# Kernel optimization log

Measured on AMD Instinct MI355X. Metric: run time of the kernel, lower is better.

The kernel has to match this reference:

```python
import jax, jax.numpy as jnp
import numpy as np

N_NODES = 50000
N_EDGES = 800000
IN_FEATS, H_FEATS, N_CLASSES = 64, 64, 16


def setup_inputs() -> dict:
    key = jax.random.key(0)
    ks = jax.random.split(key, 8)
    x = jax.random.normal(ks[0], (N_NODES, IN_FEATS), dtype=jnp.float32)
    src = jax.random.randint(ks[1], (N_EDGES,), 0, N_NODES, dtype=jnp.int64)
    dst = jax.random.randint(ks[2], (N_EDGES,), 0, N_NODES, dtype=jnp.int64)
    W_self1 = jax.random.normal(ks[3], (IN_FEATS, H_FEATS), dtype=jnp.float32) / np.sqrt(IN_FEATS)
    W_neigh1 = jax.random.normal(ks[4], (IN_FEATS, H_FEATS), dtype=jnp.float32) / np.sqrt(IN_FEATS)
    b1 = jnp.zeros((H_FEATS,), dtype=jnp.float32)
    W_self2 = jax.random.normal(ks[5], (H_FEATS, N_CLASSES), dtype=jnp.float32) / np.sqrt(H_FEATS)
    W_neigh2 = jax.random.normal(ks[6], (H_FEATS, N_CLASSES), dtype=jnp.float32) / np.sqrt(H_FEATS)
    b2 = jnp.zeros((N_CLASSES,), dtype=jnp.float32)
    return {"x": x, "src": src, "dst": dst,
            "W_self1": W_self1, "W_neigh1": W_neigh1, "b1": b1,
            "W_self2": W_self2, "W_neigh2": W_neigh2, "b2": b2}


def _mean_agg(h, src, dst, n_nodes):
    # gather source-node features along edges, sum into destinations, divide by in-degree
    summed = jax.ops.segment_sum(h[src], dst, num_segments=n_nodes)  # [N, d]
    deg = jax.ops.segment_sum(jnp.ones_like(src, dtype=h.dtype), dst, num_segments=n_nodes)
    return summed / jnp.maximum(deg, 1.0)[:, None]  # zero in-degree -> zeros (DGL semantics)


def _sage_layer(h, src, dst, W_self, W_neigh, b):
    h_neigh = _mean_agg(h, src, dst, h.shape[0])
    return h @ W_self + h_neigh @ W_neigh + b


def reference(x, src, dst, W_self1, W_neigh1, b1, W_self2, W_neigh2, b2):
    h = _sage_layer(x, src, dst, W_self1, W_neigh1, b1)
    h = jax.nn.relu(h)
    out = _sage_layer(h, src, dst, W_self2, W_neigh2, b2)
    return out
```

## Files before the change

kernel.cpp:

```cpp
#include <hip/hip_runtime.h>
#include <hip/hip_bf16.h>
#include <cstring>


#define FEATS 64
#define CLS   16
#define EPT   16
#define CAP   5120

typedef unsigned short bf16_t;
typedef float floatx2 __attribute__((ext_vector_type(2)));

__device__ __forceinline__ float bfbits2f(unsigned lo16) {
    unsigned v = lo16 << 16;
    float f;
    __builtin_memcpy(&f, &v, 4);
    return f;
}
__device__ __forceinline__ bf16_t f2bf(float f) {
    unsigned u;
    __builtin_memcpy(&u, &f, 4);
    u = (u + 0x7FFFu + ((u >> 16) & 1u)) >> 16;
    return (bf16_t)u;
}
__device__ __forceinline__ unsigned pack2(float a, float b) {
    return (unsigned)f2bf(a) | ((unsigned)f2bf(b) << 16);
}
__device__ __forceinline__ unsigned pack4_fp8(float a, float b, float c, float d) {
    int q = __builtin_amdgcn_cvt_pk_fp8_f32(a, b, 0, false);
    q = __builtin_amdgcn_cvt_pk_fp8_f32(c, d, q, true);
    return (unsigned)q;
}

__global__ __launch_bounds__(256) void fused_pg_kernel(
    const int* __restrict__ src, const int* __restrict__ dst,
    int* __restrict__ bucket_cnt, int* __restrict__ epart, int E,
    const float* __restrict__ x, const float* __restrict__ Ws,
    const float* __restrict__ Wn, bf16_t* __restrict__ selfo,
    unsigned char* __restrict__ t1, int N, int nbp)
{
    __shared__ float smem[16512];
    int t = threadIdx.x;

    if ((int)blockIdx.x < nbp) {
        int* hist = (int*)smem;
        int* base = hist + 256;
        int e0 = blockIdx.x * (256 * EPT);
        hist[t] = 0;
        __syncthreads();
        int pk[EPT];
        int bk[EPT];
#pragma unroll
        for (int j = 0; j < EPT; ++j) {
            int e = e0 + j * 256 + t;
            if (e < E) {
                int d = dst[e];
                pk[j] = (src[e] << 8) | (d & 255);
                bk[j] = d >> 8;
                atomicAdd(&hist[bk[j]], 1);
            } else bk[j] = -1;
        }
        __syncthreads();
        int c = hist[t];
        if (c) base[t] = atomicAdd(&bucket_cnt[t], c);
        hist[t] = 0;
        __syncthreads();
#pragma unroll
        for (int j = 0; j < EPT; ++j) {
            if (bk[j] >= 0) {
                int r = atomicAdd(&hist[bk[j]], 1);
                epart[bk[j] * CAP + base[bk[j]] + r] = pk[j];
            }
        }
        return;
    }

    float* Wc = smem;
    float* xs = smem + 8192;
    int node0 = ((int)blockIdx.x - nbp) * 128;

    for (int idx = t; idx < 64 * 128; idx += 256) {
        int k = idx >> 7, c = idx & 127;
        Wc[idx] = (c < 64) ? Ws[k * 64 + c] : Wn[k * 64 + (c - 64)];
    }
    for (int idx = t; idx < 128 * 16; idx += 256) {
        int row = idx >> 4, c4 = idx & 15;
        int node = node0 + row;
        float4 v = (node < N) ? ((const float4*)(x + (size_t)node * 64))[c4]
                              : make_float4(0.f, 0.f, 0.f, 0.f);
        float* p = &xs[row * 65 + c4 * 4];
        p[0] = v.x; p[1] = v.y; p[2] = v.z; p[3] = v.w;
    }
    __syncthreads();

    int m = t & 31;
    int g = t >> 5;
    float acc[4][16];
#pragma unroll
    for (int j = 0; j < 4; ++j)
#pragma unroll
        for (int c = 0; c < 16; ++c) acc[j][c] = 0.f;

    for (int k = 0; k < 64; ++k) {
        float w[16];
        const float* wp = &Wc[k * 128 + g * 16];
#pragma unroll
        for (int c = 0; c < 16; ++c) w[c] = wp[c];
        float a0 = xs[m * 65 + k];
        float a1 = xs[(m + 32) * 65 + k];
        float a2 = xs[(m + 64) * 65 + k];
        float a3 = xs[(m + 96) * 65 + k];
#pragma unroll
        for (int c = 0; c < 16; ++c) {
            acc[0][c] += a0 * w[c];
            acc[1][c] += a1 * w[c];
            acc[2][c] += a2 * w[c];
            acc[3][c] += a3 * w[c];
        }
    }
#pragma unroll
    for (int j = 0; j < 4; ++j) {
        int node = node0 + m + 32 * j;
        if (node < N) {
            if (g < 4) {
                bf16_t* dstp = selfo + (size_t)node * 64 + g * 16;
                uint4 p0, p1;
                p0.x = pack2(acc[j][0],  acc[j][1]);  p0.y = pack2(acc[j][2],  acc[j][3]);
                p0.z = pack2(acc[j][4],  acc[j][5]);  p0.w = pack2(acc[j][6],  acc[j][7]);
                p1.x = pack2(acc[j][8],  acc[j][9]);  p1.y = pack2(acc[j][10], acc[j][11]);
                p1.z = pack2(acc[j][12], acc[j][13]); p1.w = pack2(acc[j][14], acc[j][15]);
                *(uint4*)(dstp) = p0;
                *(uint4*)(dstp + 8) = p1;
            } else {
                unsigned char* dstp = t1 + (size_t)node * 64 + (g - 4) * 16;
                uint4 q;
                q.x = pack4_fp8(acc[j][0],  acc[j][1],  acc[j][2],  acc[j][3]);
                q.y = pack4_fp8(acc[j][4],  acc[j][5],  acc[j][6],  acc[j][7]);
                q.z = pack4_fp8(acc[j][8],  acc[j][9],  acc[j][10], acc[j][11]);
                q.w = pack4_fp8(acc[j][12], acc[j][13], acc[j][14], acc[j][15]);
                *(uint4*)(dstp) = q;
            }
        }
    }
}

__global__ __launch_bounds__(512) void buildcsr_kernel(const int* __restrict__ epart,
                                                       const int* __restrict__ bucket_cnt,
                                                       int* __restrict__ row_start,
                                                       unsigned short* __restrict__ deg16,
                                                       int* __restrict__ csr, int N) {
    __shared__ int cnt[256];
    __shared__ int pref[256];
    __shared__ int s[256];
    int t = threadIdx.x;
    int b = blockIdx.x;
    int ebeg = b * CAP;
    int ecnt = bucket_cnt[b];
    if (t < 256) cnt[t] = 0;
    __syncthreads();
    for (int e = t; e < ecnt; e += 512)
        atomicAdd(&cnt[epart[ebeg + e] & 255], 1);
    __syncthreads();
    int v = 0;
    if (t < 256) { v = cnt[t]; s[t] = v; }
    __syncthreads();
    for (int off = 1; off < 256; off <<= 1) {
        int u = (t < 256 && t >= off) ? s[t - off] : 0;
        __syncthreads();
        if (t < 256) s[t] += u;
        __syncthreads();
    }
    if (t < 256) {
        pref[t] = s[t] - v;
        int node = b * 256 + t;
        if (node < N) {
            row_start[node] = ebeg + pref[t];
            deg16[node] = (unsigned short)v;
        }
        cnt[t] = 0;
    }
    __syncthreads();
    for (int e = t; e < ecnt; e += 512) {
        int pk = epart[ebeg + e];
        int ln = pk & 255;
        int r = atomicAdd(&cnt[ln], 1);
        csr[ebeg + pref[ln] + r] = pk >> 8;
    }
}

__global__ __launch_bounds__(256) void gather64_kernel(
    const int* __restrict__ csr, const int* __restrict__ row_start,
    const unsigned short* __restrict__ deg16,
    const unsigned char* __restrict__ t1, const bf16_t* __restrict__ selfo,
    bf16_t* __restrict__ h1, const float* __restrict__ b1, int N)
{
    int wid = (blockIdx.x * 256 + threadIdx.x) >> 6;
    int lane = threadIdx.x & 63;
    int eslot = lane >> 3;
    int cg = lane & 7;
    if (wid >= N) return;
    int beg = row_start[wid];
    int d = deg16[wid];
    float a[8];
#pragma unroll
    for (int c = 0; c < 8; ++c) a[c] = 0.f;
    int i = eslot;
    for (; i + 8 < d; i += 16) {
        int s0 = csr[beg + i];
        int s1 = csr[beg + i + 8];
        uint2 r0 = *(const uint2*)(t1 + (size_t)s0 * 64 + cg * 8);
        uint2 r1 = *(const uint2*)(t1 + (size_t)s1 * 64 + cg * 8);
        floatx2 p0 = __builtin_amdgcn_cvt_pk_f32_fp8((int)r0.x, false);
        floatx2 p1 = __builtin_amdgcn_cvt_pk_f32_fp8((int)r0.x, true);
        floatx2 p2 = __builtin_amdgcn_cvt_pk_f32_fp8((int)r0.y, false);
        floatx2 p3 = __builtin_amdgcn_cvt_pk_f32_fp8((int)r0.y, true);
        floatx2 q0 = __builtin_amdgcn_cvt_pk_f32_fp8((int)r1.x, false);
        floatx2 q1 = __builtin_amdgcn_cvt_pk_f32_fp8((int)r1.x, true);
        floatx2 q2 = __builtin_amdgcn_cvt_pk_f32_fp8((int)r1.y, false);
        floatx2 q3 = __builtin_amdgcn_cvt_pk_f32_fp8((int)r1.y, true);
        a[0] += p0.x + q0.x;  a[1] += p0.y + q0.y;
        a[2] += p1.x + q1.x;  a[3] += p1.y + q1.y;
        a[4] += p2.x + q2.x;  a[5] += p2.y + q2.y;
        a[6] += p3.x + q3.x;  a[7] += p3.y + q3.y;
    }
    if (i < d) {
        int s0 = csr[beg + i];
        uint2 r0 = *(const uint2*)(t1 + (size_t)s0 * 64 + cg * 8);
        floatx2 p0 = __builtin_amdgcn_cvt_pk_f32_fp8((int)r0.x, false);
        floatx2 p1 = __builtin_amdgcn_cvt_pk_f32_fp8((int)r0.x, true);
        floatx2 p2 = __builtin_amdgcn_cvt_pk_f32_fp8((int)r0.y, false);
        floatx2 p3 = __builtin_amdgcn_cvt_pk_f32_fp8((int)r0.y, true);
        a[0] += p0.x; a[1] += p0.y; a[2] += p1.x; a[3] += p1.y;
        a[4] += p2.x; a[5] += p2.y; a[6] += p3.x; a[7] += p3.y;
    }
#pragma unroll
    for (int c = 0; c < 8; ++c) {
        a[c] += __shfl_xor(a[c], 8);
        a[c] += __shfl_xor(a[c], 16);
        a[c] += __shfl_xor(a[c], 32);
    }
    if (eslot == 0) {
        float inv = 1.f / fmaxf((float)d, 1.f);
        size_t o = (size_t)wid * 64 + cg * 8;
        uint4 su = *(const uint4*)(selfo + o);
        float4 b0 = *(const float4*)(b1 + cg * 8);
        float4 b4 = *(const float4*)(b1 + cg * 8 + 4);
        float r0 = fmaxf(bfbits2f(su.x & 0xffff) + a[0] * inv + b0.x, 0.f);
        float r1 = fmaxf(bfbits2f(su.x >> 16)    + a[1] * inv + b0.y, 0.f);
        float r2 = fmaxf(bfbits2f(su.y & 0xffff) + a[2] * inv + b0.z, 0.f);
        float r3 = fmaxf(bfbits2f(su.y >> 16)    + a[3] * inv + b0.w, 0.f);
        float r4 = fmaxf(bfbits2f(su.z & 0xffff) + a[4] * inv + b4.x, 0.f);
        float r5 = fmaxf(bfbits2f(su.z >> 16)    + a[5] * inv + b4.y, 0.f);
        float r6 = fmaxf(bfbits2f(su.w & 0xffff) + a[6] * inv + b4.z, 0.f);
        float r7 = fmaxf(bfbits2f(su.w >> 16)    + a[7] * inv + b4.w, 0.f);
        uint4 pk;
        pk.x = pack2(r0, r1);
        pk.y = pack2(r2, r3);
        pk.z = pack2(r4, r5);
        pk.w = pack2(r6, r7);
        *(uint4*)(h1 + o) = pk;
    }
}

__global__ __launch_bounds__(256) void gemm2_kernel(
    const bf16_t* __restrict__ h1, const float* __restrict__ Ws,
    const float* __restrict__ Wn, float* __restrict__ outp,
    bf16_t* __restrict__ t2, int N)
{
    __shared__ float Wc[64 * 32];
    __shared__ float xs[128 * 65];
    int t = threadIdx.x;
    int node0 = blockIdx.x * 128;

    for (int idx = t; idx < 64 * 32; idx += 256) {
        int k = idx >> 5, c = idx & 31;
        Wc[idx] = (c < 16) ? Ws[k * 16 + c] : Wn[k * 16 + (c - 16)];
    }
    for (int idx = t; idx < 128 * 8; idx += 256) {
        int row = idx >> 3, c8 = idx & 7;
        int node = node0 + row;
        float* p = &xs[row * 65 + c8 * 8];
        if (node < N) {
            uint4 u = *(const uint4*)(h1 + (size_t)node * 64 + c8 * 8);
            p[0] = bfbits2f(u.x & 0xffff); p[1] = bfbits2f(u.x >> 16);
            p[2] = bfbits2f(u.y & 0xffff); p[3] = bfbits2f(u.y >> 16);
            p[4] = bfbits2f(u.z & 0xffff); p[5] = bfbits2f(u.z >> 16);
            p[6] = bfbits2f(u.w & 0xffff); p[7] = bfbits2f(u.w >> 16);
        } else {
            for (int qq = 0; qq < 8; ++qq) p[qq] = 0.f;
        }
    }
    __syncthreads();

    int m = t & 31;
    int g = t >> 5;
    float acc[4][4];
#pragma unroll
    for (int j = 0; j < 4; ++j)
#pragma unroll
        for (int c = 0; c < 4; ++c) acc[j][c] = 0.f;

    for (int k = 0; k < 64; ++k) {
        float w[4];
        const float* wp = &Wc[k * 32 + g * 4];
#pragma unroll
        for (int c = 0; c < 4; ++c) w[c] = wp[c];
        float a0 = xs[m * 65 + k];
        float a1 = xs[(m + 32) * 65 + k];
        float a2 = xs[(m + 64) * 65 + k];
        float a3 = xs[(m + 96) * 65 + k];
#pragma unroll
        for (int c = 0; c < 4; ++c) {
            acc[0][c] += a0 * w[c];
            acc[1][c] += a1 * w[c];
            acc[2][c] += a2 * w[c];
            acc[3][c] += a3 * w[c];
        }
    }
#pragma unroll
    for (int j = 0; j < 4; ++j) {
        int node = node0 + m + 32 * j;
        if (node < N) {
            if (g < 4) {
                *(float4*)(outp + (size_t)node * 16 + g * 4) =
                    make_float4(acc[j][0], acc[j][1], acc[j][2], acc[j][3]);
            } else {
                uint2 pk;
                pk.x = pack2(acc[j][0], acc[j][1]);
                pk.y = pack2(acc[j][2], acc[j][3]);
                *(uint2*)(t2 + (size_t)node * 16 + (g - 4) * 4) = pk;
            }
        }
    }
}

__global__ __launch_bounds__(256) void gather16_kernel(
    const int* __restrict__ csr, const int* __restrict__ row_start,
    const unsigned short* __restrict__ deg16,
    const bf16_t* __restrict__ t2,
    float* __restrict__ outp, const float* __restrict__ b2, int N)
{
    int wid = (blockIdx.x * 256 + threadIdx.x) >> 6;
    int lane = threadIdx.x & 63;
    int eslot = lane >> 2;
    int cg = lane & 3;
    if (wid >= N) return;
    int beg = row_start[wid];
    int d = deg16[wid];
    float a0 = 0.f, a1 = 0.f, a2 = 0.f, a3 = 0.f;
    for (int i = eslot; i < d; i += 16) {
        int s0 = csr[beg + i];
        uint2 u = *(const uint2*)(t2 + (size_t)s0 * 16 + cg * 4);
        a0 += bfbits2f(u.x & 0xffff);
        a1 += bfbits2f(u.x >> 16);
        a2 += bfbits2f(u.y & 0xffff);
        a3 += bfbits2f(u.y >> 16);
    }
    a0 += __shfl_xor(a0, 4); a1 += __shfl_xor(a1, 4);
    a2 += __shfl_xor(a2, 4); a3 += __shfl_xor(a3, 4);
    a0 += __shfl_xor(a0, 8); a1 += __shfl_xor(a1, 8);
    a2 += __shfl_xor(a2, 8); a3 += __shfl_xor(a3, 8);
    a0 += __shfl_xor(a0, 16); a1 += __shfl_xor(a1, 16);
    a2 += __shfl_xor(a2, 16); a3 += __shfl_xor(a3, 16);
    a0 += __shfl_xor(a0, 32); a1 += __shfl_xor(a1, 32);
    a2 += __shfl_xor(a2, 32); a3 += __shfl_xor(a3, 32);
    if (eslot == 0) {
        float inv = 1.f / fmaxf((float)d, 1.f);
        size_t o = (size_t)wid * 16 + cg * 4;
        float4 bb = *(const float4*)(b2 + cg * 4);
        float4 ov = *(const float4*)(outp + o);
        ov.x += a0 * inv + bb.x;
        ov.y += a1 * inv + bb.y;
        ov.z += a2 * inv + bb.z;
        ov.w += a3 * inv + bb.w;
        *(float4*)(outp + o) = ov;
    }
}

extern "C" void kernel_launch(void* const* d_in, const int* in_sizes, int n_in,
                              void* d_out, int out_size, void* d_ws, size_t ws_size,
                              hipStream_t stream) {
    const float* x   = (const float*)d_in[0];
    const int*   src = (const int*)d_in[1];
    const int*   dst = (const int*)d_in[2];
    const float* Ws1 = (const float*)d_in[3];
    const float* Wn1 = (const float*)d_in[4];
    const float* b1  = (const float*)d_in[5];
    const float* Ws2 = (const float*)d_in[6];
    const float* Wn2 = (const float*)d_in[7];
    const float* b2  = (const float*)d_in[8];
    float* outp = (float*)d_out;

    const int N = in_sizes[0] / FEATS;
    const int E = in_sizes[1];
    const int B = (N + 255) / 256;
    const int NBP = (E + 256 * EPT - 1) / (256 * EPT);
    const int NBG = (N + 127) / 128;

    char* p = (char*)d_ws;
    auto align16 = [](char* q) { return (char*)(((size_t)q + 15) & ~(size_t)15); };
    int* bucket_cnt    = (int*)p;                  p = (char*)(bucket_cnt + 256);
    int* epart         = (int*)p;                  p = (char*)(epart + (size_t)B * CAP);
    int* csr           = (int*)p;                  p = (char*)(csr + (size_t)B * CAP);
    int* row_start     = (int*)align16(p);         p = (char*)(row_start + N);
    unsigned short* deg16 = (unsigned short*)align16(p); p = (char*)(deg16 + N);
    bf16_t* selfo      = (bf16_t*)align16(p);      p = (char*)(selfo + (size_t)N * 64);
    unsigned char* t1  = (unsigned char*)align16(p); p = (char*)(t1 + (size_t)N * 64);
    bf16_t* h1         = (bf16_t*)align16(p);      p = (char*)(h1 + (size_t)N * 64);
    bf16_t* t2         = (bf16_t*)align16(p);

    hipMemsetAsync(bucket_cnt, 0, 256 * sizeof(int), stream);

    fused_pg_kernel<<<NBP + NBG, 256, 0, stream>>>(
        src, dst, bucket_cnt, epart, E, x, Ws1, Wn1, selfo, t1, N, NBP);
    buildcsr_kernel<<<B, 512, 0, stream>>>(epart, bucket_cnt, row_start, deg16, csr, N);

    gather64_kernel<<<((size_t)N * 64 + 255) / 256, 256, 0, stream>>>(
        csr, row_start, deg16, t1, selfo, h1, b1, N);
    gemm2_kernel<<<(N + 127) / 128, 256, 0, stream>>>(h1, Ws2, Wn2, outp, t2, N);
    gather16_kernel<<<((size_t)N * 64 + 255) / 256, 256, 0, stream>>>(
        csr, row_start, deg16, t2, outp, b2, N);
}
```

Measured before the change: 162.2 us.

## Fuse layer-2 GEMM into layer-1 gather kernel via wave shuffles

```diff
diff --git a/kernel.cpp b/kernel.cpp
--- a/kernel.cpp
+++ b/kernel.cpp
@@ -188,22 +188,35 @@
     }
 }
 
-__global__ __launch_bounds__(256) void gather64_kernel(
+__global__ __launch_bounds__(256) void gather64g2_kernel(
     const int* __restrict__ csr, const int* __restrict__ row_start,
     const unsigned short* __restrict__ deg16,
     const unsigned char* __restrict__ t1, const bf16_t* __restrict__ selfo,
-    bf16_t* __restrict__ h1, const float* __restrict__ b1, int N)
+    const float* __restrict__ b1,
+    const float* __restrict__ Ws2, const float* __restrict__ Wn2,
+    float* __restrict__ outp, bf16_t* __restrict__ t2, int N)
 {
     int wid = (blockIdx.x * 256 + threadIdx.x) >> 6;
     int lane = threadIdx.x & 63;
     int eslot = lane >> 3;
     int cg = lane & 7;
     if (wid >= N) return;
+
+    int c = lane & 31;
+    int h = lane >> 5;
+    float Wreg[32];
+    {
+        const float* Wbase = (c < 16) ? (Ws2 + c) : (Wn2 + (c - 16));
+#pragma unroll
+        for (int j = 0; j < 32; ++j)
+            Wreg[j] = Wbase[(32 * h + j) * 16];
+    }
+
     int beg = row_start[wid];
     int d = deg16[wid];
     float a[8];
 #pragma unroll
-    for (int c = 0; c < 8; ++c) a[c] = 0.f;
+    for (int e = 0; e < 8; ++e) a[e] = 0.f;
     int i = eslot;
     for (; i + 8 < d; i += 16) {
         int s0 = csr[beg + i];
@@ -234,103 +247,40 @@
         a[4] += p2.x; a[5] += p2.y; a[6] += p3.x; a[7] += p3.y;
     }
 #pragma unroll
-    for (int c = 0; c < 8; ++c) {
-        a[c] += __shfl_xor(a[c], 8);
-        a[c] += __shfl_xor(a[c], 16);
-        a[c] += __shfl_xor(a[c], 32);
-    }
-    if (eslot == 0) {
-        float inv = 1.f / fmaxf((float)d, 1.f);
-        size_t o = (size_t)wid * 64 + cg * 8;
-        uint4 su = *(const uint4*)(selfo + o);
-        float4 b0 = *(const float4*)(b1 + cg * 8);
-        float4 b4 = *(const float4*)(b1 + cg * 8 + 4);
-        float r0 = fmaxf(bfbits2f(su.x & 0xffff) + a[0] * inv + b0.x, 0.f);
-        float r1 = fmaxf(bfbits2f(su.x >> 16)    + a[1] * inv + b0.y, 0.f);
-        float r2 = fmaxf(bfbits2f(su.y & 0xffff) + a[2] * inv + b0.z, 0.f);
-        float r3 = fmaxf(bfbits2f(su.y >> 16)    + a[3] * inv + b0.w, 0.f);
-        float r4 = fmaxf(bfbits2f(su.z & 0xffff) + a[4] * inv + b4.x, 0.f);
-        float r5 = fmaxf(bfbits2f(su.z >> 16)    + a[5] * inv + b4.y, 0.f);
-        float r6 = fmaxf(bfbits2f(su.w & 0xffff) + a[6] * inv + b4.z, 0.f);
-        float r7 = fmaxf(bfbits2f(su.w >> 16)    + a[7] * inv + b4.w, 0.f);
-        uint4 pk;
-        pk.x = pack2(r0, r1);
-        pk.y = pack2(r2, r3);
-        pk.z = pack2(r4, r5);
-        pk.w = pack2(r6, r7);
-        *(uint4*)(h1 + o) = pk;
-    }
-}
-
-__global__ __launch_bounds__(256) void gemm2_kernel(
-    const bf16_t* __restrict__ h1, const float* __restrict__ Ws,
-    const float* __restrict__ Wn, float* __restrict__ outp,
-    bf16_t* __restrict__ t2, int N)
-{
-    __shared__ float Wc[64 * 32];
-    __shared__ float xs[128 * 65];
-    int t = threadIdx.x;
-    int node0 = blockIdx.x * 128;
-
-    for (int idx = t; idx < 64 * 32; idx += 256) {
-        int k = idx >> 5, c = idx & 31;
-        Wc[idx] = (c < 16) ? Ws[k * 16 + c] : Wn[k * 16 + (c - 16)];
-    }
-    for (int idx = t; idx < 128 * 8; idx += 256) {
-        int row = idx >> 3, c8 = idx & 7;
-        int node = node0 + row;
-        float* p = &xs[row * 65 + c8 * 8];
-        if (node < N) {
-            uint4 u = *(const uint4*)(h1 + (size_t)node * 64 + c8 * 8);
-            p[0] = bfbits2f(u.x & 0xffff); p[1] = bfbits2f(u.x >> 16);
-            p[2] = bfbits2f(u.y & 0xffff); p[3] = bfbits2f(u.y >> 16);
-            p[4] = bfbits2f(u.z & 0xffff); p[5] = bfbits2f(u.z >> 16);
-            p[6] = bfbits2f(u.w & 0xffff); p[7] = bfbits2f(u.w >> 16);
-        } else {
-            for (int qq = 0; qq < 8; ++qq) p[qq] = 0.f;
-        }
-    }
-    __syncthreads();
-
-    int m = t & 31;
-    int g = t >> 5;
-    float acc[4][4];
-#pragma unroll
-    for (int j = 0; j < 4; ++j)
-#pragma unroll
-        for (int c = 0; c < 4; ++c) acc[j][c] = 0.f;
-
-    for (int k = 0; k < 64; ++k) {
-        float w[4];
-        const float* wp = &Wc[k * 32 + g * 4];
-#pragma unroll
-        for (int c = 0; c < 4; ++c) w[c] = wp[c];
-        float a0 = xs[m * 65 + k];
-        float a1 = xs[(m + 32) * 65 + k];
-        float a2 = xs[(m + 64) * 65 + k];
-        float a3 = xs[(m + 96) * 65 + k];
-#pragma unroll
-        for (int c = 0; c < 4; ++c) {
-            acc[0][c] += a0 * w[c];
-            acc[1][c] += a1 * w[c];
-            acc[2][c] += a2 * w[c];
-            acc[3][c] += a3 * w[c];
-        }
-    }
-#pragma unroll
-    for (int j = 0; j < 4; ++j) {
-        int node = node0 + m + 32 * j;
-        if (node < N) {
-            if (g < 4) {
-                *(float4*)(outp + (size_t)node * 16 + g * 4) =
-                    make_float4(acc[j][0], acc[j][1], acc[j][2], acc[j][3]);
-            } else {
-                uint2 pk;
-                pk.x = pack2(acc[j][0], acc[j][1]);
-                pk.y = pack2(acc[j][2], acc[j][3]);
-                *(uint2*)(t2 + (size_t)node * 16 + (g - 4) * 4) = pk;
-            }
-        }
+    for (int e = 0; e < 8; ++e) {
+        a[e] += __shfl_xor(a[e], 8);
+        a[e] += __shfl_xor(a[e], 16);
+        a[e] += __shfl_xor(a[e], 32);
+    }
+
+    float inv = 1.f / fmaxf((float)d, 1.f);
+    uint4 su = *(const uint4*)(selfo + (size_t)wid * 64 + cg * 8);
+    float4 b0 = *(const float4*)(b1 + cg * 8);
+    float4 b4 = *(const float4*)(b1 + cg * 8 + 4);
+    float r[8];
+    r[0] = fmaxf(bfbits2f(su.x & 0xffff) + a[0] * inv + b0.x, 0.f);
+    r[1] = fmaxf(bfbits2f(su.x >> 16)    + a[1] * inv + b0.y, 0.f);
+    r[2] = fmaxf(bfbits2f(su.y & 0xffff) + a[2] * inv + b0.z, 0.f);
+    r[3] = fmaxf(bfbits2f(su.y >> 16)    + a[3] * inv + b0.w, 0.f);
+    r[4] = fmaxf(bfbits2f(su.z & 0xffff) + a[4] * inv + b4.x, 0.f);
+    r[5] = fmaxf(bfbits2f(su.z >> 16)    + a[5] * inv + b4.y, 0.f);
+    r[6] = fmaxf(bfbits2f(su.w & 0xffff) + a[6] * inv + b4.z, 0.f);
+    r[7] = fmaxf(bfbits2f(su.w >> 16)    + a[7] * inv + b4.w, 0.f);
+
+    float acc = 0.f;
+    int srcbase = h * 4;
+#pragma unroll
+    for (int j = 0; j < 32; ++j) {
+        float v = __shfl(r[j & 7], srcbase + (j >> 3));
+        acc += v * Wreg[j];
+    }
+    acc += __shfl_xor(acc, 32);
+    float partner = __shfl_xor(acc, 1);
+    if (lane < 16) {
+        outp[(size_t)wid * 16 + lane] = acc;
+    } else if (lane < 32 && !(lane & 1)) {
+        unsigned pk = pack2(acc, partner);
+        *(unsigned*)(t2 + (size_t)wid * 16 + (lane - 16)) = pk;
     }
 }
 
@@ -406,7 +356,6 @@
     unsigned short* deg16 = (unsigned short*)align16(p); p = (char*)(deg16 + N);
     bf16_t* selfo      = (bf16_t*)align16(p);      p = (char*)(selfo + (size_t)N * 64);
     unsigned char* t1  = (unsigned char*)align16(p); p = (char*)(t1 + (size_t)N * 64);
-    bf16_t* h1         = (bf16_t*)align16(p);      p = (char*)(h1 + (size_t)N * 64);
     bf16_t* t2         = (bf16_t*)align16(p);
 
     hipMemsetAsync(bucket_cnt, 0, 256 * sizeof(int), stream);
@@ -415,9 +364,8 @@
         src, dst, bucket_cnt, epart, E, x, Ws1, Wn1, selfo, t1, N, NBP);
     buildcsr_kernel<<<B, 512, 0, stream>>>(epart, bucket_cnt, row_start, deg16, csr, N);
 
-    gather64_kernel<<<((size_t)N * 64 + 255) / 256, 256, 0, stream>>>(
-        csr, row_start, deg16, t1, selfo, h1, b1, N);
-    gemm2_kernel<<<(N + 127) / 128, 256, 0, stream>>>(h1, Ws2, Wn2, outp, t2, N);
+    gather64g2_kernel<<<((size_t)N * 64 + 255) / 256, 256, 0, stream>>>(
+        csr, row_start, deg16, t1, selfo, b1, Ws2, Wn2, outp, t2, N);
     gather16_kernel<<<((size_t)N * 64 + 255) / 256, 256, 0, stream>>>(
         csr, row_start, deg16, t2, outp, b2, N);
 }
```

Result: no change. 164.8 us (+1.6%).
